# Kernel optimization log

Measured on AMD Instinct MI355X. Metric: run time of the kernel, lower is better.

The kernel has to match this reference:

```python
import math
import jax, jax.numpy as jnp
import numpy as np

K = 4            # ensemble size
S_CONST = 0.25   # isotropic gaussian scale constant
GAUSS_DIM = 6

def pixel_shuffle(x, r):
    B, C, H, W = x.shape
    C2 = C // (r * r)
    x = x.reshape(B, C2, r, r, H, W).transpose(0, 1, 4, 2, 5, 3)
    return x.reshape(B, C2, H * r, W * r)

def pixel_unshuffle(x, r):
    B, C, H, W = x.shape
    x = x.reshape(B, C, H // r, r, W // r, r).transpose(0, 1, 3, 5, 2, 4)
    return x.reshape(B, C * r * r, H // r, W // r)

def setup_inputs():
    key = jax.random.key(0)
    k1, k2, k3 = jax.random.split(key, 3)
    B, h, w = 4, 128, 128
    inp = jax.random.normal(k1, (B, 3, h, w), jnp.float32)
    w_enc = jax.random.normal(k2, (1024, 3, 3, 3), jnp.float32) * 0.05
    b_enc = jnp.zeros((1024,), jnp.float32)
    w_head = jax.random.normal(k3, (GAUSS_DIM * K, 256), jnp.float32) * 0.05
    b_head = jnp.zeros((GAUSS_DIM * K,), jnp.float32)
    return {"inp": inp, "w_enc": w_enc, "b_enc": b_enc,
            "w_head": w_head, "b_head": b_head, "scale": 2}

def _forward(inp, w_enc, b_enc, w_head, b_head, scale):
    B, _, h, w = inp.shape
    s1 = s2 = float(scale)
    H, W = round(h * s1), round(w * s2)
    # --- encoder (conv3x3 -> pixel_shuffle x4 -> 64ch @ 4h x 4w) ---
    x = jax.lax.conv_general_dilated(inp, w_enc, (1, 1), 'SAME',
        dimension_numbers=('NCHW', 'OIHW', 'NCHW')) + b_enc[None, :, None, None]
    x = pixel_shuffle(x, 4)                 # [B, 64, 4h, 4w]
    feat = pixel_unshuffle(x, 2)            # [B, 256, 2h, 2w]
    # --- gauss head (1x1 conv) ---
    pred_map = jnp.einsum('bchw,oc->bohw', feat, w_head) + b_head[None, :, None, None]
    gh, gw = 2 * h, 2 * w
    N = gh * gw
    pred = pred_map.reshape(B, GAUSS_DIM * K, N).transpose(0, 2, 1).reshape(B, N, K, GAUSS_DIM)
    rgb_k, off_raw, w_logits = pred[..., :3], pred[..., 3:5], pred[..., 5:6]
    wgt = jax.nn.softmax(w_logits, axis=2)
    rgb = (rgb_k * wgt).sum(2)              # [B, N, 3]
    off = (jnp.tanh(off_raw) * wgt).sum(2)  # [B, N, 2]
    # --- gaussian centers in NDC ---
    yi, xi = jnp.meshgrid(jnp.arange(gh), jnp.arange(gw), indexing='ij')
    coordx = (xi / gw * 2.0 - 1.0).reshape(-1).astype(jnp.float32)
    coordy = (yi / gh * 2.0 - 1.0).reshape(-1).astype(jnp.float32)
    x_ndc = coordx[None, :] + 2.0 * off[..., 0] / w - 1.0 / W
    y_ndc = coordy[None, :] + 2.0 * off[..., 1] / h - 1.0 / H
    # --- rasterize: isotropic gaussians, local 3-sigma window, scatter-add ---
    s_px = S_CONST * s1                     # pixel-space std (theta = 0)
    r = max(2, int(math.ceil(3.0 * s_px)))
    offs = jnp.arange(-r, r + 1)

    def raster_one(xn, yn, col):
        cx = 0.5 * ((xn + 1.0) * W - 1.0)   # ndc -> pixel center
        cy = 0.5 * ((yn + 1.0) * H - 1.0)
        px = jnp.floor(cx)[:, None] + offs  # [N, 2r+1]
        py = jnp.floor(cy)[:, None] + offs
        dx = px - cx[:, None]
        dy = py - cy[:, None]
        power = -0.5 * (dy[:, :, None] ** 2 + dx[:, None, :] ** 2) / (s_px * s_px)
        alpha = jnp.minimum(0.999, jnp.exp(power))
        alpha = jnp.where(alpha > 1.0 / 255.0, alpha, 0.0)   # kernel alpha cutoff
        pxi = px.astype(jnp.int32)
        pyi = py.astype(jnp.int32)
        valid = ((pyi[:, :, None] >= 0) & (pyi[:, :, None] < H) &
                 (pxi[:, None, :] >= 0) & (pxi[:, None, :] < W))
        contrib = jnp.where(valid, alpha, 0.0)               # [N, wy, wx]
        yfull = jnp.clip(jnp.broadcast_to(pyi[:, :, None], contrib.shape), 0, H - 1)
        xfull = jnp.clip(jnp.broadcast_to(pxi[:, None, :], contrib.shape), 0, W - 1)
        img = jnp.zeros((H, W, 3), jnp.float32).at[yfull, xfull].add(
            contrib[..., None] * col[:, None, None, :])
        return jnp.clip(img, 0.0, 1.0).transpose(2, 0, 1)    # [3, H, W]

    return jax.vmap(raster_one)(x_ndc, y_ndc, rgb)

def reference(inp, w_enc, b_enc, w_head, b_head, scale):
    return _forward(inp, w_enc, b_enc, w_head, b_head, scale)
```

## Files before the change

kernel.cpp:

```cpp
#include <hip/hip_runtime.h>
#include <math.h>

#define NB 4
#define IH 128
#define IW 128
#define GH 256
#define GW 256

#define TSX 16
#define TSY 32
#define GRX 24
#define GRY 40
#define NG (GRX * GRY)

#define WEFF_FLOATS (4 * 24 * 27)
#define BEFF_FLOATS (4 * 24)

__device__ __forceinline__ float fast_tanh(float x) {
  return 1.f - 2.f / (__expf(2.f * x) + 1.f);
}
__device__ __forceinline__ float clamp01(float v) {
  return fminf(1.f, fmaxf(0.f, v));
}

__global__ __launch_bounds__(256) void weff_kernel(
    const float* __restrict__ w_enc, const float* __restrict__ b_enc,
    const float* __restrict__ w_head, const float* __restrict__ b_head,
    float* __restrict__ weff, float* __restrict__ beff) {
  __shared__ float sWH[24 * 256];
  __shared__ float sWE[256 * 27];
  __shared__ float sBE[256];

  int tid = (int)threadIdx.x;
  int p = (int)blockIdx.x;
  int ph = p >> 1, pw = p & 1;

  for (int i = tid; i < 24 * 256; i += 256) sWH[i] = w_head[i];
  {
    int hc = tid;
    int ch = ((hc >> 2) << 4) + (2 * ph + ((hc >> 1) & 1)) * 4 + (2 * pw + (hc & 1));
    for (int t = 0; t < 27; ++t) sWE[hc * 27 + t] = w_enc[ch * 27 + t];
    sBE[hc] = b_enc[ch];
  }
  __syncthreads();

  for (int j = tid; j < 24 * 27; j += 256) {
    int o = j / 27, t = j % 27;
    float a = 0.f;
    for (int hc = 0; hc < 256; ++hc) a = fmaf(sWH[o * 256 + hc], sWE[hc * 27 + t], a);
    weff[p * (24 * 27) + j] = a;
  }
  if (tid < 24) {
    float a = b_head[tid];
    for (int hc = 0; hc < 256; ++hc) a = fmaf(sWH[tid * 256 + hc], sBE[hc], a);
    beff[p * 24 + tid] = a;
  }
}

__global__ __launch_bounds__(256) void gather_kernel(
    const float* __restrict__ inp, const float* __restrict__ weff,
    const float* __restrict__ beff, float* __restrict__ out) {
  __shared__ float sW[WEFF_FLOATS];
  __shared__ float sB[BEFF_FLOATS];
  __shared__ float sCC[NG * 2];
  __shared__ float4 sCol[NG];

  int tid = (int)threadIdx.x;
  for (int i = tid; i < WEFF_FLOATS; i += 256) sW[i] = weff[i];
  for (int i = tid; i < BEFF_FLOATS; i += 256) sB[i] = beff[i];
  __syncthreads();

  int bid = (int)blockIdx.x;
  int b = bid >> 7;
  int t = bid & 127;
  int TY = (t >> 4) * TSY;
  int TX = (t & 15) * TSX;
  const float* ib = inp + b * 3 * IH * IW;

  for (int gi = tid; gi < NG; gi += 256) {
    int gyr = gi / GRX, gxr = gi - gyr * GRX;
    int hh = TY - 3 + gyr, ww = TX - 3 + gxr;
    if ((unsigned)hh < GH && (unsigned)ww < GW) {
      int ph = hh & 1, pw_ = ww & 1, p = ph * 2 + pw_;
      int hs = hh >> 1, ws_ = ww >> 1;

      float in[27];
      #pragma unroll
      for (int cin = 0; cin < 3; ++cin) {
        #pragma unroll
        for (int ky = 0; ky < 3; ++ky) {
          int y = hs + ky - 1;
          #pragma unroll
          for (int kx = 0; kx < 3; ++kx) {
            int x = ws_ + kx - 1;
            float v = 0.f;
            if (y >= 0 && y < IH && x >= 0 && x < IW) v = ib[(cin * IH + y) * IW + x];
            in[cin * 9 + ky * 3 + kx] = v;
          }
        }
      }

      float pr[24];
      #pragma unroll
      for (int o = 0; o < 24; ++o) {
        float a = sB[p * 24 + o];
        const float* w = &sW[(p * 24 + o) * 27];
        #pragma unroll
        for (int k = 0; k < 27; ++k) a = fmaf(in[k], w[k], a);
        pr[o] = a;
      }

      float l0 = pr[5], l1 = pr[11], l2 = pr[17], l3 = pr[23];
      float m = fmaxf(fmaxf(l0, l1), fmaxf(l2, l3));
      float e0 = __expf(l0 - m), e1 = __expf(l1 - m);
      float e2 = __expf(l2 - m), e3 = __expf(l3 - m);
      float inv = 1.f / (e0 + e1 + e2 + e3);
      float w0 = e0 * inv, w1 = e1 * inv, w2 = e2 * inv, w3 = e3 * inv;
      float cr = w0 * pr[0] + w1 * pr[6] + w2 * pr[12] + w3 * pr[18];
      float cg = w0 * pr[1] + w1 * pr[7] + w2 * pr[13] + w3 * pr[19];
      float cb = w0 * pr[2] + w1 * pr[8] + w2 * pr[14] + w3 * pr[20];
      float ox = w0 * fast_tanh(pr[3]) + w1 * fast_tanh(pr[9]) +
                 w2 * fast_tanh(pr[15]) + w3 * fast_tanh(pr[21]);
      float oy = w0 * fast_tanh(pr[4]) + w1 * fast_tanh(pr[10]) +
                 w2 * fast_tanh(pr[16]) + w3 * fast_tanh(pr[22]);

      float coordx = ((float)ww / 256.f) * 2.f - 1.f;
      float coordy = ((float)hh / 256.f) * 2.f - 1.f;
      float x_ndc = coordx + 2.f * ox / 128.f - 1.f / 256.f;
      float y_ndc = coordy + 2.f * oy / 128.f - 1.f / 256.f;
      float cx = 0.5f * ((x_ndc + 1.f) * 256.f - 1.f);
      float cy = 0.5f * ((y_ndc + 1.f) * 256.f - 1.f);

      sCC[gi * 2] = cy;
      sCC[gi * 2 + 1] = cx;
      sCol[gi] = float4{cr, cg, cb, 0.f};
    } else {
      sCC[gi * 2] = 1e9f;
      sCC[gi * 2 + 1] = 1e9f;
      sCol[gi] = float4{0.f, 0.f, 0.f, 0.f};
    }
  }
  __syncthreads();

  int pxl = tid & 15;
  int pyl = (tid >> 4) * 2;
  int px = TX + pxl, py = TY + pyl;
  float fpx = (float)px, fpy0 = (float)py, fpy1 = fpy0 + 1.f;

  float r0 = 0.f, g0 = 0.f, b0 = 0.f;
  float r1 = 0.f, g1 = 0.f, b1 = 0.f;

  for (int ry = 0; ry < 10; ++ry) {
    int gb = (pyl + ry) * GRX + pxl;
    #pragma unroll
    for (int rx = 0; rx < 9; ++rx) {
      int g = gb + rx;
      float cyv = sCC[g * 2];
      float cxv = sCC[g * 2 + 1];
      float dx = fpx - cxv;
      float dy0 = fpy0 - cyv;
      float dy1 = fpy1 - cyv;
      float dx2 = dx * dx;
      float rr0 = fmaf(dy0, dy0, dx2);
      float rr1 = fmaf(dy1, dy1, dx2);
      float a0 = fminf(0.999f, __expf(-2.f * rr0));
      float a1 = fminf(0.999f, __expf(-2.f * rr1));
      a0 = (a0 > (1.f / 255.f)) ? a0 : 0.f;
      a1 = (a1 > (1.f / 255.f)) ? a1 : 0.f;
      if (a0 + a1 > 0.f) {
        float4 c = sCol[g];
        r0 = fmaf(a0, c.x, r0); g0 = fmaf(a0, c.y, g0); b0 = fmaf(a0, c.z, b0);
        r1 = fmaf(a1, c.x, r1); g1 = fmaf(a1, c.y, g1); b1 = fmaf(a1, c.z, b1);
      }
    }
  }

  float* ob = out + b * 3 * GH * GW;
  int i0 = py * GW + px;
  int i1 = i0 + GW;
  ob[i0] = clamp01(r0);
  ob[GH * GW + i0] = clamp01(g0);
  ob[2 * GH * GW + i0] = clamp01(b0);
  ob[i1] = clamp01(r1);
  ob[GH * GW + i1] = clamp01(g1);
  ob[2 * GH * GW + i1] = clamp01(b1);
}

extern "C" void kernel_launch(void* const* d_in, const int* in_sizes, int n_in,
                              void* d_out, int out_size, void* d_ws, size_t ws_size,
                              hipStream_t stream) {
  const float* inp = (const float*)d_in[0];
  const float* w_enc = (const float*)d_in[1];
  const float* b_enc = (const float*)d_in[2];
  const float* w_head = (const float*)d_in[3];
  const float* b_head = (const float*)d_in[4];

  float* weff = (float*)d_ws;
  float* beff = weff + WEFF_FLOATS;

  weff_kernel<<<4, 256, 0, stream>>>(w_enc, b_enc, w_head, b_head, weff, beff);

  gather_kernel<<<NB * 128, 256, 0, stream>>>(inp, weff, beff, (float*)d_out);
}
```

Before: 113.0 us.

## Split gaussian prediction into separate kernel to remove halo recomputation

The fused gather kernel recomputed gaussian parameters for a haloed region per tile, so overlapping halos were computed several times. Gaussian parameters (centers and colors) are now computed exactly once per gaussian in a new kernel, two per thread sharing weight loads, and written to workspace. A smaller-tile gather kernel then reads the haloed region from global memory and rasterises one pixel per thread. It uses a squared-radius cutoff test instead of computing exp first, so exp only runs for in-range gaussians. The cost is an extra launch and a global round trip of about 20 bytes per gaussian.

```diff
diff --git a/kernel.cpp b/kernel.cpp
--- a/kernel.cpp
+++ b/kernel.cpp
@@ -6,15 +6,21 @@
 #define IW 128
 #define GH 256
 #define GW 256
-
-#define TSX 16
-#define TSY 32
-#define GRX 24
-#define GRY 40
-#define NG (GRX * GRY)
+#define NGAUSS (NB * GH * GW)
 
 #define WEFF_FLOATS (4 * 24 * 27)
 #define BEFF_FLOATS (4 * 24)
+#define POS_OFF 2688
+#define CR_OFF (POS_OFF + 2 * NGAUSS)
+#define CG_OFF (CR_OFF + NGAUSS)
+#define CB_OFF (CG_OFF + NGAUSS)
+
+#define TSX 16
+#define TSY 16
+#define GR 24
+#define NREG (GR * GR)
+#define RR_MAX 2.770360f
+#define EXP2C (-2.8853900818f)
 
 __device__ __forceinline__ float fast_tanh(float x) {
   return 1.f - 2.f / (__expf(2.f * x) + 1.f);
@@ -57,133 +63,163 @@
   }
 }
 
-__global__ __launch_bounds__(256) void gather_kernel(
-    const float* __restrict__ inp, const float* __restrict__ weff,
-    const float* __restrict__ beff, float* __restrict__ out) {
-  __shared__ float sW[WEFF_FLOATS];
+__global__ __launch_bounds__(256) void gauss_kernel(
+    const float* __restrict__ inp, const float* __restrict__ ws_ro,
+    float* __restrict__ ws) {
+  __shared__ float sW[4 * 24 * 28];
   __shared__ float sB[BEFF_FLOATS];
-  __shared__ float sCC[NG * 2];
-  __shared__ float4 sCol[NG];
 
   int tid = (int)threadIdx.x;
-  for (int i = tid; i < WEFF_FLOATS; i += 256) sW[i] = weff[i];
-  for (int i = tid; i < BEFF_FLOATS; i += 256) sB[i] = beff[i];
+  for (int i = tid; i < 4 * 24 * 28; i += 256) {
+    int row = i / 28, k = i - row * 28;
+    sW[i] = (k < 27) ? ws_ro[row * 27 + k] : 0.f;
+  }
+  for (int i = tid; i < BEFF_FLOATS; i += 256) sB[i] = ws_ro[WEFF_FLOATS + i];
   __syncthreads();
 
   int bid = (int)blockIdx.x;
   int b = bid >> 7;
   int t = bid & 127;
+  int TYg = (t >> 3) * 16;
+  int TXg = (t & 7) * 32;
+  int hh = TYg + (tid >> 4);
+  int ww0 = TXg + (tid & 15);
+  int p = (hh & 1) * 2 + (ww0 & 1);
+  int hs = hh >> 1, ws0 = ww0 >> 1;
+
+  const float* ib = inp + b * 3 * IH * IW;
+  float in0[28], in1[28];
+  in0[27] = 0.f; in1[27] = 0.f;
+  #pragma unroll
+  for (int cin = 0; cin < 3; ++cin) {
+    #pragma unroll
+    for (int ky = 0; ky < 3; ++ky) {
+      int y = hs + ky - 1;
+      bool yok = (y >= 0 && y < IH);
+      #pragma unroll
+      for (int kx = 0; kx < 3; ++kx) {
+        int x0 = ws0 + kx - 1;
+        int x1 = x0 + 8;
+        float v0 = 0.f, v1 = 0.f;
+        if (yok && x0 >= 0 && x0 < IW) v0 = ib[(cin * IH + y) * IW + x0];
+        if (yok && x1 < IW) v1 = ib[(cin * IH + y) * IW + x1];
+        in0[cin * 9 + ky * 3 + kx] = v0;
+        in1[cin * 9 + ky * 3 + kx] = v1;
+      }
+    }
+  }
+
+  float a0[24], a1[24];
+  #pragma unroll
+  for (int o = 0; o < 24; ++o) { float bi = sB[p * 24 + o]; a0[o] = bi; a1[o] = bi; }
+  #pragma unroll
+  for (int o = 0; o < 24; ++o) {
+    const float4* wrow = (const float4*)&sW[(p * 24 + o) * 28];
+    #pragma unroll
+    for (int kq = 0; kq < 7; ++kq) {
+      float4 w = wrow[kq];
+      a0[o] = fmaf(in0[kq * 4 + 0], w.x, a0[o]);
+      a0[o] = fmaf(in0[kq * 4 + 1], w.y, a0[o]);
+      a0[o] = fmaf(in0[kq * 4 + 2], w.z, a0[o]);
+      a0[o] = fmaf(in0[kq * 4 + 3], w.w, a0[o]);
+      a1[o] = fmaf(in1[kq * 4 + 0], w.x, a1[o]);
+      a1[o] = fmaf(in1[kq * 4 + 1], w.y, a1[o]);
+      a1[o] = fmaf(in1[kq * 4 + 2], w.z, a1[o]);
+      a1[o] = fmaf(in1[kq * 4 + 3], w.w, a1[o]);
+    }
+  }
+
+  float2* posP = (float2*)(ws + POS_OFF);
+
+  #pragma unroll
+  for (int which = 0; which < 2; ++which) {
+    const float* pr = which ? a1 : a0;
+    int ww = which ? (ww0 + 16) : ww0;
+
+    float l0 = pr[5], l1 = pr[11], l2 = pr[17], l3 = pr[23];
+    float m = fmaxf(fmaxf(l0, l1), fmaxf(l2, l3));
+    float e0 = __expf(l0 - m), e1 = __expf(l1 - m);
+    float e2 = __expf(l2 - m), e3 = __expf(l3 - m);
+    float inv = 1.f / (e0 + e1 + e2 + e3);
+    float w0 = e0 * inv, w1 = e1 * inv, w2 = e2 * inv, w3 = e3 * inv;
+    float cr = w0 * pr[0] + w1 * pr[6] + w2 * pr[12] + w3 * pr[18];
+    float cg = w0 * pr[1] + w1 * pr[7] + w2 * pr[13] + w3 * pr[19];
+    float cb = w0 * pr[2] + w1 * pr[8] + w2 * pr[14] + w3 * pr[20];
+    float ox = w0 * fast_tanh(pr[3]) + w1 * fast_tanh(pr[9]) +
+               w2 * fast_tanh(pr[15]) + w3 * fast_tanh(pr[21]);
+    float oy = w0 * fast_tanh(pr[4]) + w1 * fast_tanh(pr[10]) +
+               w2 * fast_tanh(pr[16]) + w3 * fast_tanh(pr[22]);
+
+    float coordx = ((float)ww / 256.f) * 2.f - 1.f;
+    float coordy = ((float)hh / 256.f) * 2.f - 1.f;
+    float x_ndc = coordx + 2.f * ox / 128.f - 1.f / 256.f;
+    float y_ndc = coordy + 2.f * oy / 128.f - 1.f / 256.f;
+    float cx = 0.5f * ((x_ndc + 1.f) * 256.f - 1.f);
+    float cy = 0.5f * ((y_ndc + 1.f) * 256.f - 1.f);
+
+    int g = (b << 16) | (hh << 8) | ww;
+    posP[g] = make_float2(cy, cx);
+    ws[CR_OFF + g] = cr;
+    ws[CG_OFF + g] = cg;
+    ws[CB_OFF + g] = cb;
+  }
+}
+
+__global__ __launch_bounds__(256) void gather_kernel(
+    const float* __restrict__ ws, float* __restrict__ out) {
+  __shared__ float2 sPos[NREG];
+  __shared__ float4 sCol[NREG];
+
+  int tid = (int)threadIdx.x;
+  int bid = (int)blockIdx.x;
+  int b = bid >> 8;
+  int t = bid & 255;
   int TY = (t >> 4) * TSY;
   int TX = (t & 15) * TSX;
-  const float* ib = inp + b * 3 * IH * IW;
-
-  for (int gi = tid; gi < NG; gi += 256) {
-    int gyr = gi / GRX, gxr = gi - gyr * GRX;
-    int hh = TY - 3 + gyr, ww = TX - 3 + gxr;
+  const float2* posP = (const float2*)(ws + POS_OFF);
+
+  for (int i = tid; i < NREG; i += 256) {
+    int r = i / GR, c = i - r * GR;
+    int hh = TY - 3 + r, ww = TX - 3 + c;
     if ((unsigned)hh < GH && (unsigned)ww < GW) {
-      int ph = hh & 1, pw_ = ww & 1, p = ph * 2 + pw_;
-      int hs = hh >> 1, ws_ = ww >> 1;
-
-      float in[27];
-      #pragma unroll
-      for (int cin = 0; cin < 3; ++cin) {
-        #pragma unroll
-        for (int ky = 0; ky < 3; ++ky) {
-          int y = hs + ky - 1;
-          #pragma unroll
-          for (int kx = 0; kx < 3; ++kx) {
-            int x = ws_ + kx - 1;
-            float v = 0.f;
-            if (y >= 0 && y < IH && x >= 0 && x < IW) v = ib[(cin * IH + y) * IW + x];
-            in[cin * 9 + ky * 3 + kx] = v;
-          }
-        }
+      int g = (b << 16) | (hh << 8) | ww;
+      sPos[i] = posP[g];
+      sCol[i] = make_float4(ws[CR_OFF + g], ws[CG_OFF + g], ws[CB_OFF + g], 0.f);
+    } else {
+      sPos[i] = make_float2(1e9f, 1e9f);
+      sCol[i] = make_float4(0.f, 0.f, 0.f, 0.f);
+    }
+  }
+  __syncthreads();
+
+  int pxl = tid & 15, pyl = tid >> 4;
+  float fpx = (float)(TX + pxl), fpy = (float)(TY + pyl);
+  float ar = 0.f, ag = 0.f, ab = 0.f;
+
+  #pragma unroll
+  for (int ry = 0; ry < 8; ++ry) {
+    int base = (pyl + ry) * GR + pxl;
+    #pragma unroll
+    for (int rx = 0; rx < 8; ++rx) {
+      float2 P = sPos[base + rx];
+      float dy = fpy - P.x;
+      float dx = fpx - P.y;
+      float rr = fmaf(dy, dy, dx * dx);
+      if (rr < RR_MAX) {
+        float al = fminf(0.999f, exp2f(EXP2C * rr));
+        float4 C = sCol[base + rx];
+        ar = fmaf(al, C.x, ar);
+        ag = fmaf(al, C.y, ag);
+        ab = fmaf(al, C.z, ab);
       }
-
-      float pr[24];
-      #pragma unroll
-      for (int o = 0; o < 24; ++o) {
-        float a = sB[p * 24 + o];
-        const float* w = &sW[(p * 24 + o) * 27];
-        #pragma unroll
-        for (int k = 0; k < 27; ++k) a = fmaf(in[k], w[k], a);
-        pr[o] = a;
-      }
-
-      float l0 = pr[5], l1 = pr[11], l2 = pr[17], l3 = pr[23];
-      float m = fmaxf(fmaxf(l0, l1), fmaxf(l2, l3));
-      float e0 = __expf(l0 - m), e1 = __expf(l1 - m);
-      float e2 = __expf(l2 - m), e3 = __expf(l3 - m);
-      float inv = 1.f / (e0 + e1 + e2 + e3);
-      float w0 = e0 * inv, w1 = e1 * inv, w2 = e2 * inv, w3 = e3 * inv;
-      float cr = w0 * pr[0] + w1 * pr[6] + w2 * pr[12] + w3 * pr[18];
-      float cg = w0 * pr[1] + w1 * pr[7] + w2 * pr[13] + w3 * pr[19];
-      float cb = w0 * pr[2] + w1 * pr[8] + w2 * pr[14] + w3 * pr[20];
-      float ox = w0 * fast_tanh(pr[3]) + w1 * fast_tanh(pr[9]) +
-                 w2 * fast_tanh(pr[15]) + w3 * fast_tanh(pr[21]);
-      float oy = w0 * fast_tanh(pr[4]) + w1 * fast_tanh(pr[10]) +
-                 w2 * fast_tanh(pr[16]) + w3 * fast_tanh(pr[22]);
-
-      float coordx = ((float)ww / 256.f) * 2.f - 1.f;
-      float coordy = ((float)hh / 256.f) * 2.f - 1.f;
-      float x_ndc = coordx + 2.f * ox / 128.f - 1.f / 256.f;
-      float y_ndc = coordy + 2.f * oy / 128.f - 1.f / 256.f;
-      float cx = 0.5f * ((x_ndc + 1.f) * 256.f - 1.f);
-      float cy = 0.5f * ((y_ndc + 1.f) * 256.f - 1.f);
-
-      sCC[gi * 2] = cy;
-      sCC[gi * 2 + 1] = cx;
-      sCol[gi] = float4{cr, cg, cb, 0.f};
-    } else {
-      sCC[gi * 2] = 1e9f;
-      sCC[gi * 2 + 1] = 1e9f;
-      sCol[gi] = float4{0.f, 0.f, 0.f, 0.f};
-    }
-  }
-  __syncthreads();
-
-  int pxl = tid & 15;
-  int pyl = (tid >> 4) * 2;
-  int px = TX + pxl, py = TY + pyl;
-  float fpx = (float)px, fpy0 = (float)py, fpy1 = fpy0 + 1.f;
-
-  float r0 = 0.f, g0 = 0.f, b0 = 0.f;
-  float r1 = 0.f, g1 = 0.f, b1 = 0.f;
-
-  for (int ry = 0; ry < 10; ++ry) {
-    int gb = (pyl + ry) * GRX + pxl;
-    #pragma unroll
-    for (int rx = 0; rx < 9; ++rx) {
-      int g = gb + rx;
-      float cyv = sCC[g * 2];
-      float cxv = sCC[g * 2 + 1];
-      float dx = fpx - cxv;
-      float dy0 = fpy0 - cyv;
-      float dy1 = fpy1 - cyv;
-      float dx2 = dx * dx;
-      float rr0 = fmaf(dy0, dy0, dx2);
-      float rr1 = fmaf(dy1, dy1, dx2);
-      float a0 = fminf(0.999f, __expf(-2.f * rr0));
-      float a1 = fminf(0.999f, __expf(-2.f * rr1));
-      a0 = (a0 > (1.f / 255.f)) ? a0 : 0.f;
-      a1 = (a1 > (1.f / 255.f)) ? a1 : 0.f;
-      if (a0 + a1 > 0.f) {
-        float4 c = sCol[g];
-        r0 = fmaf(a0, c.x, r0); g0 = fmaf(a0, c.y, g0); b0 = fmaf(a0, c.z, b0);
-        r1 = fmaf(a1, c.x, r1); g1 = fmaf(a1, c.y, g1); b1 = fmaf(a1, c.z, b1);
-      }
     }
   }
 
   float* ob = out + b * 3 * GH * GW;
-  int i0 = py * GW + px;
-  int i1 = i0 + GW;
-  ob[i0] = clamp01(r0);
-  ob[GH * GW + i0] = clamp01(g0);
-  ob[2 * GH * GW + i0] = clamp01(b0);
-  ob[i1] = clamp01(r1);
-  ob[GH * GW + i1] = clamp01(g1);
-  ob[2 * GH * GW + i1] = clamp01(b1);
+  int i0 = (TY + pyl) * GW + (TX + pxl);
+  ob[i0] = clamp01(ar);
+  ob[GH * GW + i0] = clamp01(ag);
+  ob[2 * GH * GW + i0] = clamp01(ab);
 }
 
 extern "C" void kernel_launch(void* const* d_in, const int* in_sizes, int n_in,
@@ -195,10 +231,13 @@
   const float* w_head = (const float*)d_in[3];
   const float* b_head = (const float*)d_in[4];
 
-  float* weff = (float*)d_ws;
-  float* beff = weff + WEFF_FLOATS;
+  float* ws = (float*)d_ws;
+  float* weff = ws;
+  float* beff = ws + WEFF_FLOATS;
 
   weff_kernel<<<4, 256, 0, stream>>>(w_enc, b_enc, w_head, b_head, weff, beff);
 
-  gather_kernel<<<NB * 128, 256, 0, stream>>>(inp, weff, beff, (float*)d_out);
-}
+  gauss_kernel<<<512, 256, 0, stream>>>(inp, ws, ws);
+
+  gather_kernel<<<NB * 256, 256, 0, stream>>>(ws, (float*)d_out);
+}
```

Result: faster. 100.8 us (-10.8%).
